# Kernel optimization log

Hardware: AMD Instinct MI355X
Metric: run time of the kernel (lower is better)

Reference implementation:

```python
import jax, jax.numpy as jnp
import numpy as np

NUM_POSITIONS = 4096
EMBED_DIM = 512
BSZ, SEQ_LEN = 16, 4096


def setup_inputs() -> dict:
    key = jax.random.key(0)
    k1, k2 = jax.random.split(key)
    input_tensor = jax.random.normal(k1, (BSZ, SEQ_LEN, EMBED_DIM), dtype=jnp.float32)
    pv = jax.random.normal(k2, (NUM_POSITIONS, EMBED_DIM), dtype=jnp.float32)
    # L2-normalize each position vector (as in _init_position_vectors)
    pv = pv / jnp.linalg.norm(pv, axis=1, keepdims=True)
    return {"input_tensor": input_tensor, "position_vectors": pv}


def reference(input_tensor, position_vectors):
    # input_tensor: [B, S, D]; position_vectors: [P, D] with S <= P.
    seq_len, d = input_tensor.shape[1], input_tensor.shape[-1]
    pos = position_vectors[:seq_len]  # [S, D]
    # Batched circular convolution over the last axis via rFFT.
    x_fft = jnp.fft.rfft(input_tensor, axis=-1)          # [B, S, D//2+1] complex
    p_fft = jnp.fft.rfft(pos, axis=-1)[None, :, :]       # [1, S, D//2+1]
    out = jnp.fft.irfft(x_fft * p_fft, n=d, axis=-1)     # [B, S, D]
    return out.astype(input_tensor.dtype)
```

## Files before the change

### kernel.cpp

```cpp
#include <hip/hip_runtime.h>
#include <math.h>

#ifndef M_PI
#define M_PI 3.14159265358979323846
#endif

#define SEQ 4096
#define DIM 512

#define REG_SZ 624

#define TOTAL_ITEMS (SEQ*8)
#define NW 8192
#define ITERS (TOTAL_ITEMS/NW)

__device__ __forceinline__ void wsync(){
  asm volatile("s_waitcnt lgkmcnt(0)" ::: "memory");
  __builtin_amdgcn_wave_barrier();
}

__device__ __forceinline__ float2 cadd(float2 a, float2 b){ return make_float2(a.x+b.x, a.y+b.y); }
__device__ __forceinline__ float2 csub(float2 a, float2 b){ return make_float2(a.x-b.x, a.y-b.y); }
__device__ __forceinline__ float2 cmul(float2 a, float2 b){
  return make_float2(fmaf(a.x, b.x, -(a.y*b.y)), fmaf(a.x, b.y, a.y*b.x));
}
__device__ __forceinline__ float2 cmulc(float2 a, float2 b){
  return make_float2(fmaf(a.x, b.x, a.y*b.y), fmaf(a.y, b.x, -(a.x*b.y)));
}
__device__ __forceinline__ float2 mul_mi(float2 a){ return make_float2(a.y, -a.x); }

__device__ __forceinline__ void dft8(const float2* in, float2* out){
  float2 t0 = cadd(in[0], in[4]), t1 = csub(in[0], in[4]);
  float2 t2 = cadd(in[2], in[6]), t3 = csub(in[2], in[6]);
  float2 E0 = cadd(t0, t2), E2 = csub(t0, t2);
  float2 m3 = mul_mi(t3);
  float2 E1 = cadd(t1, m3), E3 = csub(t1, m3);
  float2 s0 = cadd(in[1], in[5]), s1 = csub(in[1], in[5]);
  float2 s2 = cadd(in[3], in[7]), s3 = csub(in[3], in[7]);
  float2 O0 = cadd(s0, s2), O2 = csub(s0, s2);
  float2 n3 = mul_mi(s3);
  float2 O1 = cadd(s1, n3), O3 = csub(s1, n3);
  const float C = 0.70710678118654752440f;
  float2 w1o = make_float2(C*(O1.x + O1.y), C*(O1.y - O1.x));
  float2 w2o = mul_mi(O2);
  float2 w3o = make_float2(C*(O3.y - O3.x), -(C*(O3.x + O3.y)));
  out[0] = cadd(E0, O0); out[4] = csub(E0, O0);
  out[1] = cadd(E1, w1o); out[5] = csub(E1, w1o);
  out[2] = cadd(E2, w2o); out[6] = csub(E2, w2o);
  out[3] = cadd(E3, w3o); out[7] = csub(E3, w3o);
}

__device__ __forceinline__ void idft8(const float2* in, float2* out){
  float2 t[8];
  dft8(in, t);
  out[0]=t[0]; out[1]=t[7]; out[2]=t[6]; out[3]=t[5];
  out[4]=t[4]; out[5]=t[3]; out[6]=t[2]; out[7]=t[1];
}

__device__ __forceinline__ void make_twiddles(int lane, float2* wA, float2* wB){
  const int b = lane & 7;
  float sv, cv;
  sincosf(-2.0f*(float)M_PI*(float)lane*(1.0f/512.0f), &sv, &cv);
  const float2 a1 = make_float2(cv, sv);
  sincosf(-2.0f*(float)M_PI*(float)b*(1.0f/64.0f), &sv, &cv);
  const float2 b1 = make_float2(cv, sv);
  wA[0] = make_float2(1.f, 0.f); wB[0] = make_float2(1.f, 0.f);
  wA[1] = a1; wB[1] = b1;
  #pragma unroll
  for (int r = 2; r < 8; ++r){ wA[r] = cmul(wA[r-1], a1); wB[r] = cmul(wB[r-1], b1); }
}

__device__ __forceinline__ void fft512_fwd(float2* v, float2* lds, int lane,
                                           const float2* wA, const float2* wB){
  const int a = lane >> 3, b = lane & 7;
  float2 t[8];
  dft8(v, t);
  #pragma unroll
  for (int r = 1; r < 8; ++r) t[r] = cmul(t[r], wA[r]);
  #pragma unroll
  for (int r = 0; r < 8; ++r) lds[72*r + lane] = t[r];
  wsync();
  #pragma unroll
  for (int j2 = 0; j2 < 8; ++j2) v[j2] = lds[72*a + b + 8*j2];
  dft8(v, t);
  #pragma unroll
  for (int r2 = 1; r2 < 8; ++r2) t[r2] = cmul(t[r2], wB[r2]);
  #pragma unroll
  for (int r2 = 0; r2 < 8; ++r2) lds[a + 78*r2 + 10*b] = t[r2];
  wsync();
  #pragma unroll
  for (int i2 = 0; i2 < 8; ++i2) v[i2] = lds[a + 78*b + 10*i2];
  dft8(v, t);
  #pragma unroll
  for (int m = 0; m < 8; ++m) v[m] = t[m];
}

__device__ __forceinline__ void fft512_inv(float2* v, float2* lds, int lane,
                                           const float2* wA, const float2* wB){
  const int a = lane >> 3, b = lane & 7;
  float2 t[8];
  idft8(v, t);
  #pragma unroll
  for (int i2 = 0; i2 < 8; ++i2) lds[a + 78*b + 10*i2] = t[i2];
  wsync();
  #pragma unroll
  for (int r2 = 0; r2 < 8; ++r2) v[r2] = lds[a + 78*r2 + 10*b];
  #pragma unroll
  for (int r2 = 1; r2 < 8; ++r2) v[r2] = cmulc(v[r2], wB[r2]);
  idft8(v, t);
  #pragma unroll
  for (int j2 = 0; j2 < 8; ++j2) lds[72*a + b + 8*j2] = t[j2];
  wsync();
  #pragma unroll
  for (int r = 0; r < 8; ++r) v[r] = lds[72*r + lane];
  #pragma unroll
  for (int r = 1; r < 8; ++r) v[r] = cmulc(v[r], wA[r]);
  idft8(v, t);
  #pragma unroll
  for (int j = 0; j < 8; ++j) v[j] = t[j];
}

__global__ void __launch_bounds__(256)
pfft_kernel(const float* __restrict__ p, float2* __restrict__ pspec){
  __shared__ float2 lds_all[4 * REG_SZ];
  const int lane = threadIdx.x & 63;
  const int wid  = threadIdx.x >> 6;
  float2* lds = lds_all + wid * REG_SZ;
  const int s = blockIdx.x * 4 + wid;

  float2 wA[8], wB[8];
  make_twiddles(lane, wA, wB);

  const float* prow = p + (size_t)s * DIM;
  float2 pf[8];
  #pragma unroll
  for (int j = 0; j < 8; ++j) pf[j] = make_float2(prow[lane + 64*j], 0.f);
  fft512_fwd(pf, lds, lane, wA, wB);
  #pragma unroll
  for (int m = 0; m < 8; ++m){
    pf[m].x *= (1.0f/512.0f); pf[m].y *= (1.0f/512.0f);
    pspec[(size_t)s * DIM + 64*m + lane] = pf[m];
  }
}

__global__ void __launch_bounds__(128)
circconv_kernel(const float* __restrict__ x, const float2* __restrict__ pspec,
                float* __restrict__ out){
  __shared__ float2 lds_all[2 * REG_SZ];
  const int lane = threadIdx.x & 63;
  const int wid  = threadIdx.x >> 6;
  float2* lds = lds_all + wid * REG_SZ;

  const int wg = blockIdx.x * 2 + wid;
  const size_t row_stride = (size_t)SEQ * DIM;

  float2 wA[8], wB[8];
  make_twiddles(lane, wA, wB);

  int item = wg;
  size_t b0 = ((size_t)(2*(item & 7)) * SEQ + (item >> 3)) * DIM;
  size_t b1 = b0 + row_stride;
  float pre0[8], pre1[8];
  #pragma unroll
  for (int j = 0; j < 8; ++j){
    pre0[j] = x[b0 + lane + 64*j];
    pre1[j] = x[b1 + lane + 64*j];
  }

  #pragma unroll 1
  for (int it = 0; it < ITERS; ++it){
    const int s = item >> 3;
    const size_t cb0 = b0, cb1 = b1;

    float2 v[8];
    #pragma unroll
    for (int j = 0; j < 8; ++j) v[j] = make_float2(pre0[j], pre1[j]);

    float2 pf[8];
    #pragma unroll
    for (int m = 0; m < 8; ++m) pf[m] = pspec[(size_t)s * DIM + 64*m + lane];

    if (it + 1 < ITERS){
      const int ni = item + NW;
      b0 = ((size_t)(2*(ni & 7)) * SEQ + (ni >> 3)) * DIM;
      b1 = b0 + row_stride;
      #pragma unroll
      for (int j = 0; j < 8; ++j){
        pre0[j] = x[b0 + lane + 64*j];
        pre1[j] = x[b1 + lane + 64*j];
      }
      item = ni;
    }

    fft512_fwd(v, lds, lane, wA, wB);
    #pragma unroll
    for (int m = 0; m < 8; ++m) v[m] = cmul(v[m], pf[m]);
    fft512_inv(v, lds, lane, wA, wB);

    #pragma unroll
    for (int j = 0; j < 8; ++j){
      out[cb0 + lane + 64*j] = v[j].x;
      out[cb1 + lane + 64*j] = v[j].y;
    }
  }
}

__global__ void __launch_bounds__(256)
circconv_fallback_kernel(const float* __restrict__ x, const float* __restrict__ p,
                         float* __restrict__ out){
  __shared__ float2 lds_all[4 * REG_SZ];
  const int lane = threadIdx.x & 63;
  const int wid  = threadIdx.x >> 6;
  float2* lds = lds_all + wid * REG_SZ;

  const int g    = blockIdx.x * 4 + wid;
  const int s    = g >> 1;
  const int half = g & 1;

  float2 wA[8], wB[8];
  make_twiddles(lane, wA, wB);

  float2 pf[8];
  {
    const float* prow = p + (size_t)s * DIM;
    #pragma unroll
    for (int j = 0; j < 8; ++j) pf[j] = make_float2(prow[lane + 64*j], 0.f);
    fft512_fwd(pf, lds, lane, wA, wB);
    #pragma unroll
    for (int m = 0; m < 8; ++m){ pf[m].x *= (1.0f/512.0f); pf[m].y *= (1.0f/512.0f); }
  }

  const size_t row_stride = (size_t)SEQ * DIM;
  const int b_lo = half * 8;
  for (int bb = b_lo; bb < b_lo + 8; bb += 2){
    const size_t base0 = ((size_t)bb * SEQ + s) * DIM;
    const size_t base1 = base0 + row_stride;
    float2 v[8];
    #pragma unroll
    for (int j = 0; j < 8; ++j)
      v[j] = make_float2(x[base0 + lane + 64*j], x[base1 + lane + 64*j]);
    fft512_fwd(v, lds, lane, wA, wB);
    #pragma unroll
    for (int m = 0; m < 8; ++m) v[m] = cmul(v[m], pf[m]);
    fft512_inv(v, lds, lane, wA, wB);
    #pragma unroll
    for (int j = 0; j < 8; ++j){
      out[base0 + lane + 64*j] = v[j].x;
      out[base1 + lane + 64*j] = v[j].y;
    }
  }
}

extern "C" void kernel_launch(void* const* d_in, const int* in_sizes, int n_in,
                              void* d_out, int out_size, void* d_ws, size_t ws_size,
                              hipStream_t stream) {
  (void)in_sizes; (void)n_in; (void)out_size;
  const float* x  = (const float*)d_in[0];
  const float* p  = (const float*)d_in[1];
  float* o        = (float*)d_out;

  const size_t pspec_bytes = (size_t)SEQ * DIM * sizeof(float2);
  if (ws_size >= pspec_bytes){
    float2* pspec = (float2*)d_ws;
    pfft_kernel<<<SEQ/4, 256, 0, stream>>>(p, pspec);
    circconv_kernel<<<NW/2, 128, 0, stream>>>(x, pspec, o);
  } else {
    circconv_fallback_kernel<<<SEQ*2/4, 256, 0, stream>>>(x, p, o);
  }
}
```

Measured before the change: 250.4 us.

## Prefetch next input rows into LDS via async global_load_lds instead of registers

```diff
diff --git a/kernel.cpp b/kernel.cpp
--- a/kernel.cpp
+++ b/kernel.cpp
@@ -9,6 +9,7 @@
 #define DIM 512
 
 #define REG_SZ 624
+#define STG_F 1024
 
 #define TOTAL_ITEMS (SEQ*8)
 #define NW 8192
@@ -17,6 +18,15 @@
 __device__ __forceinline__ void wsync(){
   asm volatile("s_waitcnt lgkmcnt(0)" ::: "memory");
   __builtin_amdgcn_wave_barrier();
+}
+__device__ __forceinline__ void vwait0(){
+  asm volatile("s_waitcnt vmcnt(0)" ::: "memory");
+}
+
+__device__ __forceinline__ void async_copy16(const float* g, float* l){
+  __builtin_amdgcn_global_load_lds(
+      (const __attribute__((address_space(1))) void*)g,
+      (__attribute__((address_space(3))) void*)l, 16, 0, 0);
 }
 
 __device__ __forceinline__ float2 cadd(float2 a, float2 b){ return make_float2(a.x+b.x, a.y+b.y); }
@@ -146,61 +156,69 @@
 __global__ void __launch_bounds__(128)
 circconv_kernel(const float* __restrict__ x, const float2* __restrict__ pspec,
                 float* __restrict__ out){
-  __shared__ float2 lds_all[2 * REG_SZ];
+  __shared__ float2 lds_fft[2 * REG_SZ];
+  __shared__ float  stg_all[2 * STG_F];
   const int lane = threadIdx.x & 63;
   const int wid  = threadIdx.x >> 6;
-  float2* lds = lds_all + wid * REG_SZ;
+  float2* lds = lds_fft + wid * REG_SZ;
+  float*  stg = stg_all + wid * STG_F;
 
   const int wg = blockIdx.x * 2 + wid;
   const size_t row_stride = (size_t)SEQ * DIM;
 
+  int item = wg;
+  {
+    const size_t b0 = ((size_t)(2*(item & 7)) * SEQ + (item >> 3)) * DIM;
+    const size_t b1 = b0 + row_stride;
+    async_copy16(x + b0 +       4*lane, stg +   0);
+    async_copy16(x + b0 + 256 + 4*lane, stg + 256);
+    async_copy16(x + b1 +       4*lane, stg + 512);
+    async_copy16(x + b1 + 256 + 4*lane, stg + 768);
+  }
+
   float2 wA[8], wB[8];
   make_twiddles(lane, wA, wB);
-
-  int item = wg;
-  size_t b0 = ((size_t)(2*(item & 7)) * SEQ + (item >> 3)) * DIM;
-  size_t b1 = b0 + row_stride;
-  float pre0[8], pre1[8];
-  #pragma unroll
-  for (int j = 0; j < 8; ++j){
-    pre0[j] = x[b0 + lane + 64*j];
-    pre1[j] = x[b1 + lane + 64*j];
-  }
+  vwait0();
 
   #pragma unroll 1
   for (int it = 0; it < ITERS; ++it){
     const int s = item >> 3;
-    const size_t cb0 = b0, cb1 = b1;
+    const size_t b0 = ((size_t)(2*(item & 7)) * SEQ + s) * DIM;
+    const size_t b1 = b0 + row_stride;
 
     float2 v[8];
     #pragma unroll
-    for (int j = 0; j < 8; ++j) v[j] = make_float2(pre0[j], pre1[j]);
-
-    float2 pf[8];
-    #pragma unroll
-    for (int m = 0; m < 8; ++m) pf[m] = pspec[(size_t)s * DIM + 64*m + lane];
+    for (int j = 0; j < 8; ++j)
+      v[j] = make_float2(stg[lane + 64*j], stg[512 + lane + 64*j]);
+    wsync();
+    __builtin_amdgcn_sched_barrier(0);
 
     if (it + 1 < ITERS){
       const int ni = item + NW;
-      b0 = ((size_t)(2*(ni & 7)) * SEQ + (ni >> 3)) * DIM;
-      b1 = b0 + row_stride;
-      #pragma unroll
-      for (int j = 0; j < 8; ++j){
-        pre0[j] = x[b0 + lane + 64*j];
-        pre1[j] = x[b1 + lane + 64*j];
-      }
+      const size_t n0 = ((size_t)(2*(ni & 7)) * SEQ + (ni >> 3)) * DIM;
+      const size_t n1 = n0 + row_stride;
+      async_copy16(x + n0 +       4*lane, stg +   0);
+      async_copy16(x + n0 + 256 + 4*lane, stg + 256);
+      async_copy16(x + n1 +       4*lane, stg + 512);
+      async_copy16(x + n1 + 256 + 4*lane, stg + 768);
       item = ni;
     }
 
+    float2 pf[8];
+    #pragma unroll
+    for (int m = 0; m < 8; ++m) pf[m] = pspec[(size_t)s * DIM + 64*m + lane];
+
     fft512_fwd(v, lds, lane, wA, wB);
     #pragma unroll
     for (int m = 0; m < 8; ++m) v[m] = cmul(v[m], pf[m]);
     fft512_inv(v, lds, lane, wA, wB);
 
+    vwait0();
+
     #pragma unroll
     for (int j = 0; j < 8; ++j){
-      out[cb0 + lane + 64*j] = v[j].x;
-      out[cb1 + lane + 64*j] = v[j].y;
+      out[b0 + lane + 64*j] = v[j].x;
+      out[b1 + lane + 64*j] = v[j].y;
     }
   }
 }
```

New measurement: 251.8 us. About the same (+0.5%).
